# Performance work log

Measured on AMD Instinct MI355X. Metric: run time of the kernel, lower is better.

The kernel has to match this reference:

```python
import jax, jax.numpy as jnp
import numpy as np

B, I, H, V = 256, 512, 1024, 512


def _lstm_cell(x, h, c, W, U, b):
    # Keras LSTMCell: z = x@kernel + h@recurrent_kernel + bias, gate order i,f,g,o
    z = x @ W + h @ U + b  # [B, 4H]
    i, f, g, o = jnp.split(z, 4, axis=-1)
    i = jax.nn.sigmoid(i)
    f = jax.nn.sigmoid(f)
    g = jnp.tanh(g)
    o = jax.nn.sigmoid(o)
    c_new = f * c + i * g
    h_new = o * jnp.tanh(c_new)
    return h_new, c_new


def setup_inputs() -> dict:
    key = jax.random.key(0)
    ks = jax.random.split(key, 16)
    s_in = 1.0 / np.sqrt(I)
    s_h = 1.0 / np.sqrt(H)
    inp = {
        'x': jax.random.normal(ks[0], (B, I), jnp.float32),
        'h0': jax.random.normal(ks[1], (B, H), jnp.float32) * 0.1,
        'c0': jax.random.normal(ks[2], (B, H), jnp.float32) * 0.1,
        'h1': jax.random.normal(ks[3], (B, H), jnp.float32) * 0.1,
        'c1': jax.random.normal(ks[4], (B, H), jnp.float32) * 0.1,
        'h2': jax.random.normal(ks[5], (B, H), jnp.float32) * 0.1,
        'c2': jax.random.normal(ks[6], (B, H), jnp.float32) * 0.1,
        'W0': jax.random.normal(ks[7], (I, 4 * H), jnp.float32) * s_in,
        'U0': jax.random.normal(ks[8], (H, 4 * H), jnp.float32) * s_h,
        'b0': jnp.zeros((4 * H,), jnp.float32),
        'W1': jax.random.normal(ks[9], (H, 4 * H), jnp.float32) * s_h,
        'U1': jax.random.normal(ks[10], (H, 4 * H), jnp.float32) * s_h,
        'b1': jnp.zeros((4 * H,), jnp.float32),
        'W2': jax.random.normal(ks[11], (H, 4 * H), jnp.float32) * s_h,
        'U2': jax.random.normal(ks[12], (H, 4 * H), jnp.float32) * s_h,
        'b2': jnp.zeros((4 * H,), jnp.float32),
        'Wp': jax.random.normal(ks[13], (H, V), jnp.float32) * s_h,
        'bp': jnp.zeros((V,), jnp.float32),
    }
    return inp


def reference(x, h0, c0, h1, c1, h2, c2, W0, U0, b0, W1, U1, b1, W2, U2, b2, Wp, bp):
    # Stacked LSTM cells: output of each cell feeds the next
    h0n, c0n = _lstm_cell(x, h0, c0, W0, U0, b0)
    h1n, c1n = _lstm_cell(h0n, h1, c1, W1, U1, b1)
    h2n, c2n = _lstm_cell(h1n, h2, c2, W2, U2, b2)
    # Dense output projection on final cell output
    step_logits = h2n @ Wp + bp  # [B, V]
    return (step_logits, h0n, c0n, h1n, c1n, h2n, c2n)
```

## Files before the change

### kernel.cpp

```cpp
#include <hip/hip_runtime.h>


typedef __attribute__((ext_vector_type(8))) short short8_t;
typedef __attribute__((ext_vector_type(8))) unsigned short ushort8_t;
typedef __attribute__((ext_vector_type(4))) unsigned short ushort4_t;
typedef __attribute__((ext_vector_type(4))) float f32x4;

__device__ __forceinline__ unsigned short f2bf(float f) {
    union { float f; unsigned u; } v; v.f = f;
    unsigned r = v.u + 0x7FFFu + ((v.u >> 16) & 1u);
    return (unsigned short)(r >> 16);
}

#define KT 64

__global__ __launch_bounds__(512, 2)
void gemm32(const unsigned short* __restrict__ A1, const float* __restrict__ W1, int K1,
            const unsigned short* __restrict__ A2, const float* __restrict__ W2,
            int N, int Ktot, int nsplit, float* __restrict__ zp)
{
    __shared__ unsigned short Al0[256 * KT];
    __shared__ unsigned short Al1[256 * KT];
    __shared__ unsigned short Wl0[32 * KT];
    __shared__ unsigned short Wl1[32 * KT];

    const int tid  = threadIdx.x;
    const int lane = tid & 63;
    const int w    = tid >> 6;
    const int lg   = lane >> 4;
    const int lr   = lane & 15;
    const int bid  = blockIdx.x;
    const int kb   = bid & (nsplit - 1);
    const int ns   = bid >> (nsplit - 1);
    const int n0   = ns * 32;
    const int m0   = w * 32;
    const int klen = Ktot >> (nsplit - 1);
    const int kbeg = kb * klen;
    const int nt   = klen >> 6;

    const int wkr = tid >> 3;
    const int wcq = tid & 7;

    ushort8_t paA[4], paB[4];
    f32x4     pwA,   pwB;

    f32x4 acc00 = {0,0,0,0}, acc01 = {0,0,0,0}, acc10 = {0,0,0,0}, acc11 = {0,0,0,0};

    auto issue = [&](int t, ushort8_t (&pa)[4], f32x4& pw) {
        int k0 = kbeg + t * KT;
        const unsigned short* A; const float* Wm; int ldA, krel;
        if (k0 < K1) { A = A1; Wm = W1; ldA = K1;        krel = k0; }
        else         { A = A2; Wm = W2; ldA = Ktot - K1; krel = k0 - K1; }
#pragma unroll
        for (int it = 0; it < 4; ++it) {
            int c = tid + it * 512;
            int row = c >> 3, cc = c & 7;
            pa[it] = *(const ushort8_t*)(A + (size_t)row * ldA + krel + cc * 8);
        }
        pw = *(const f32x4*)(Wm + (size_t)(krel + wkr) * N + n0 + wcq * 4);
    };

    auto stage = [&](ushort8_t (&pa)[4], f32x4& pw,
                     unsigned short* al, unsigned short* wl) {
#pragma unroll
        for (int it = 0; it < 4; ++it) {
            int c = tid + it * 512;
            int row = c >> 3, cc = c & 7;
            *(ushort8_t*)(al + row * KT + ((cc ^ (row & 7)) << 3)) = pa[it];
        }
        unsigned short bs[4] = { f2bf(pw[0]), f2bf(pw[1]), f2bf(pw[2]), f2bf(pw[3]) };
        int kch = wkr >> 3, kwi = wkr & 7;
#pragma unroll
        for (int j = 0; j < 4; ++j) {
            int n = wcq * 4 + j;
            wl[n * KT + ((kch ^ (n & 7)) << 3) + kwi] = bs[j];
        }
    };

    auto compute = [&](const unsigned short* al, const unsigned short* wl) {
#pragma unroll
        for (int ks = 0; ks < 2; ++ks) {
            int ch = ks * 4 + lg;
            int nb0 = lr, nb1 = 16 + lr;
            short8_t b0f = *(const short8_t*)(wl + nb0 * KT + ((ch ^ (nb0 & 7)) << 3));
            short8_t b1f = *(const short8_t*)(wl + nb1 * KT + ((ch ^ (nb1 & 7)) << 3));
            int r0 = m0 + lr, r1 = m0 + 16 + lr;
            short8_t a0f = *(const short8_t*)(al + r0 * KT + ((ch ^ (r0 & 7)) << 3));
            short8_t a1f = *(const short8_t*)(al + r1 * KT + ((ch ^ (r1 & 7)) << 3));
            acc00 = __builtin_amdgcn_mfma_f32_16x16x32_bf16(a0f, b0f, acc00, 0, 0, 0);
            acc01 = __builtin_amdgcn_mfma_f32_16x16x32_bf16(a0f, b1f, acc01, 0, 0, 0);
            acc10 = __builtin_amdgcn_mfma_f32_16x16x32_bf16(a1f, b0f, acc10, 0, 0, 0);
            acc11 = __builtin_amdgcn_mfma_f32_16x16x32_bf16(a1f, b1f, acc11, 0, 0, 0);
        }
    };

    issue(0, paA, pwA);
    stage(paA, pwA, Al0, Wl0);
    issue(1, paB, pwB);
    __syncthreads();

    for (int t = 0; t < nt; t += 2) {
        if (t + 2 < nt) issue(t + 2, paA, pwA);
        stage(paB, pwB, Al1, Wl1);
        compute(Al0, Wl0);
        __syncthreads();
        if (t + 3 < nt) issue(t + 3, paB, pwB);
        if (t + 2 < nt) stage(paA, pwA, Al0, Wl0);
        compute(Al1, Wl1);
        __syncthreads();
    }

    float* zrow = zp + (size_t)kb * 256 * N;
#pragma unroll
    for (int r = 0; r < 4; ++r) {
        int ma = m0 + lg * 4 + r;
        int mb = ma + 16;
        zrow[(size_t)ma * N + n0 + lr]      = acc00[r];
        zrow[(size_t)ma * N + n0 + 16 + lr] = acc01[r];
        zrow[(size_t)mb * N + n0 + lr]      = acc10[r];
        zrow[(size_t)mb * N + n0 + 16 + lr] = acc11[r];
    }
}

__global__ __launch_bounds__(256)
void lstm_gates(const float* __restrict__ zp0, const float* __restrict__ zp1,
                const float* __restrict__ bias, const float* __restrict__ c_old,
                float* __restrict__ h_out, float* __restrict__ c_out,
                unsigned short* __restrict__ h_bf)
{
    int t = blockIdx.x * 256 + threadIdx.x;
    int b = t >> 8;
    int n = (t & 255) << 2;
    const float* z0 = zp0 + (size_t)b * 4096;
    f32x4 iv = *(const f32x4*)(z0 + n);
    f32x4 fv = *(const f32x4*)(z0 + 1024 + n);
    f32x4 gv = *(const f32x4*)(z0 + 2048 + n);
    f32x4 ov = *(const f32x4*)(z0 + 3072 + n);
    if (zp1) {
        const float* z1 = zp1 + (size_t)b * 4096;
        iv += *(const f32x4*)(z1 + n);
        fv += *(const f32x4*)(z1 + 1024 + n);
        gv += *(const f32x4*)(z1 + 2048 + n);
        ov += *(const f32x4*)(z1 + 3072 + n);
    }
    iv += *(const f32x4*)(bias + n);
    fv += *(const f32x4*)(bias + 1024 + n);
    gv += *(const f32x4*)(bias + 2048 + n);
    ov += *(const f32x4*)(bias + 3072 + n);
    f32x4 cv = *(const f32x4*)(c_old + (size_t)b * 1024 + n);

    f32x4 hn, cn;
    ushort4_t hb;
#pragma unroll
    for (int j = 0; j < 4; ++j) {
        float ii = 1.f / (1.f + __expf(-iv[j]));
        float ff = 1.f / (1.f + __expf(-fv[j]));
        float gg = tanhf(gv[j]);
        float oo = 1.f / (1.f + __expf(-ov[j]));
        float c2 = ff * cv[j] + ii * gg;
        cn[j] = c2;
        float h2 = oo * tanhf(c2);
        hn[j] = h2;
        hb[j] = f2bf(h2);
    }
    *(f32x4*)(c_out + (size_t)b * 1024 + n) = cn;
    *(f32x4*)(h_out + (size_t)b * 1024 + n) = hn;
    *(ushort4_t*)(h_bf + (size_t)b * 1024 + n) = hb;
}

__global__ __launch_bounds__(256)
void finalize_proj(const float* __restrict__ zp0, const float* __restrict__ zp1,
                   const float* __restrict__ bp, float* __restrict__ logits)
{
    int t = blockIdx.x * 256 + threadIdx.x;
    int i = t * 4;
    f32x4 v = *(const f32x4*)(zp0 + i);
    if (zp1) v += *(const f32x4*)(zp1 + i);
    v += *(const f32x4*)(bp + (i & 511));
    *(f32x4*)(logits + i) = v;
}

__global__ __launch_bounds__(256)
void pack_bf16(const float* __restrict__ x,  const float* __restrict__ h0,
               const float* __restrict__ h1, const float* __restrict__ h2,
               unsigned short* __restrict__ xb,  unsigned short* __restrict__ h0b,
               unsigned short* __restrict__ h1b, unsigned short* __restrict__ h2b)
{
    int t = blockIdx.x * 256 + threadIdx.x;
    const float* src; unsigned short* dst; int off;
    if (t < 32768)       { src = x;  dst = xb;  off = t; }
    else if (t < 98304)  { src = h0; dst = h0b; off = t - 32768; }
    else if (t < 163840) { src = h1; dst = h1b; off = t - 98304; }
    else                 { src = h2; dst = h2b; off = t - 163840; }
    f32x4 v = *(const f32x4*)(src + (size_t)off * 4);
    ushort4_t o;
#pragma unroll
    for (int j = 0; j < 4; ++j) o[j] = f2bf(v[j]);
    *(ushort4_t*)(dst + (size_t)off * 4) = o;
}

extern "C" void kernel_launch(void* const* d_in, const int* in_sizes, int n_in,
                              void* d_out, int out_size, void* d_ws, size_t ws_size,
                              hipStream_t stream)
{
    const float* x  = (const float*)d_in[0];
    const float* h0 = (const float*)d_in[1];
    const float* c0 = (const float*)d_in[2];
    const float* h1 = (const float*)d_in[3];
    const float* c1 = (const float*)d_in[4];
    const float* h2 = (const float*)d_in[5];
    const float* c2 = (const float*)d_in[6];
    const float* W0 = (const float*)d_in[7];
    const float* U0 = (const float*)d_in[8];
    const float* b0 = (const float*)d_in[9];
    const float* W1 = (const float*)d_in[10];
    const float* U1 = (const float*)d_in[11];
    const float* b1 = (const float*)d_in[12];
    const float* W2 = (const float*)d_in[13];
    const float* U2 = (const float*)d_in[14];
    const float* b2 = (const float*)d_in[15];
    const float* Wp = (const float*)d_in[16];
    const float* bp = (const float*)d_in[17];

    float* out    = (float*)d_out;
    float* logits = out;
    float* h0n = out + 131072;
    float* c0n = h0n + 262144;
    float* h1n = c0n + 262144;
    float* c1n = h1n + 262144;
    float* h2n = c1n + 262144;
    float* c2n = h2n + 262144;

    const size_t need2 = 8388608ull + 262144ull + 6ull * 524288ull;
    const int nsplit = (ws_size >= need2) ? 2 : 1;
    const size_t zbytes = (size_t)nsplit * 4194304ull;

    char* ws = (char*)d_ws;
    float*          zp   = (float*)ws;
    unsigned short* xb   = (unsigned short*)(ws + zbytes);
    unsigned short* h0b  = (unsigned short*)(ws + zbytes + 262144);
    unsigned short* h1b  = (unsigned short*)(ws + zbytes + 262144 + 524288);
    unsigned short* h2b  = (unsigned short*)(ws + zbytes + 262144 + 2*524288);
    unsigned short* h0nb = (unsigned short*)(ws + zbytes + 262144 + 3*524288);
    unsigned short* h1nb = (unsigned short*)(ws + zbytes + 262144 + 4*524288);
    unsigned short* h2nb = (unsigned short*)(ws + zbytes + 262144 + 5*524288);

    const float* zp1  = (nsplit == 2) ? zp + 1048576 : nullptr;
    const float* zpp1 = (nsplit == 2) ? zp + 131072  : nullptr;

    pack_bf16<<<896, 256, 0, stream>>>(x, h0, h1, h2, xb, h0b, h1b, h2b);

    gemm32<<<128 * nsplit, 512, 0, stream>>>(xb, W0, 512, h0b, U0, 4096, 1536, nsplit, zp);
    lstm_gates<<<256, 256, 0, stream>>>(zp, zp1, b0, c0, h0n, c0n, h0nb);

    gemm32<<<128 * nsplit, 512, 0, stream>>>(h0nb, W1, 1024, h1b, U1, 4096, 2048, nsplit, zp);
    lstm_gates<<<256, 256, 0, stream>>>(zp, zp1, b1, c1, h1n, c1n, h1nb);

    gemm32<<<128 * nsplit, 512, 0, stream>>>(h1nb, W2, 1024, h2b, U2, 4096, 2048, nsplit, zp);
    lstm_gates<<<256, 256, 0, stream>>>(zp, zp1, b2, c2, h2n, c2n, h2nb);

    gemm32<<<16 * nsplit, 512, 0, stream>>>(h2nb, Wp, 1024,
                                            (const unsigned short*)nullptr,
                                            (const float*)nullptr, 512, 1024, nsplit, zp);
    finalize_proj<<<128, 256, 0, stream>>>(zp, zpp1, bp, logits);
}
```

Measured before the change: 75.79 us.

## Widen GEMM N-tile to 64, deepen register prefetch, allow 4-way split-K

```diff
diff --git a/kernel.cpp b/kernel.cpp
--- a/kernel.cpp
+++ b/kernel.cpp
@@ -13,40 +13,43 @@
 }
 
 #define KT 64
-
-__global__ __launch_bounds__(512, 2)
-void gemm32(const unsigned short* __restrict__ A1, const float* __restrict__ W1, int K1,
+#define BN 64
+
+__global__ __launch_bounds__(512, 1)
+void gemm64(const unsigned short* __restrict__ A1, const float* __restrict__ W1, int K1,
             const unsigned short* __restrict__ A2, const float* __restrict__ W2,
-            int N, int Ktot, int nsplit, float* __restrict__ zp)
-{
-    __shared__ unsigned short Al0[256 * KT];
-    __shared__ unsigned short Al1[256 * KT];
-    __shared__ unsigned short Wl0[32 * KT];
-    __shared__ unsigned short Wl1[32 * KT];
+            int N, int Ktot, int lgs, float* __restrict__ zp)
+{
+    __shared__ unsigned short Al[2][256 * KT];
+    __shared__ unsigned short Wl[2][BN * KT];
 
     const int tid  = threadIdx.x;
     const int lane = tid & 63;
     const int w    = tid >> 6;
     const int lg   = lane >> 4;
     const int lr   = lane & 15;
-    const int bid  = blockIdx.x;
-    const int kb   = bid & (nsplit - 1);
-    const int ns   = bid >> (nsplit - 1);
-    const int n0   = ns * 32;
+    const int nsplit = 1 << lgs;
+    const int kb   = blockIdx.x & (nsplit - 1);
+    const int ns   = blockIdx.x >> lgs;
+    const int n0   = ns * BN;
     const int m0   = w * 32;
-    const int klen = Ktot >> (nsplit - 1);
+    const int klen = Ktot >> lgs;
     const int kbeg = kb * klen;
     const int nt   = klen >> 6;
 
-    const int wkr = tid >> 3;
-    const int wcq = tid & 7;
-
-    ushort8_t paA[4], paB[4];
-    f32x4     pwA,   pwB;
-
-    f32x4 acc00 = {0,0,0,0}, acc01 = {0,0,0,0}, acc10 = {0,0,0,0}, acc11 = {0,0,0,0};
-
-    auto issue = [&](int t, ushort8_t (&pa)[4], f32x4& pw) {
+    const int wr = tid >> 3;
+    const int wq = tid & 7;
+
+    ushort8_t pa0[4], pa1[4], pa2[4], pa3[4];
+    f32x4     pw0[2], pw1[2], pw2[2], pw3[2];
+
+    f32x4 acc[2][4];
+#pragma unroll
+    for (int i = 0; i < 2; ++i)
+#pragma unroll
+        for (int j = 0; j < 4; ++j) acc[i][j] = f32x4{0.f, 0.f, 0.f, 0.f};
+
+    auto issue = [&](int t, ushort8_t (&pa)[4], f32x4 (&pw)[2]) {
         int k0 = kbeg + t * KT;
         const unsigned short* A; const float* Wm; int ldA, krel;
         if (k0 < K1) { A = A1; Wm = W1; ldA = K1;        krel = k0; }
@@ -57,10 +60,12 @@
             int row = c >> 3, cc = c & 7;
             pa[it] = *(const ushort8_t*)(A + (size_t)row * ldA + krel + cc * 8);
         }
-        pw = *(const f32x4*)(Wm + (size_t)(krel + wkr) * N + n0 + wcq * 4);
+        const float* wrow = Wm + (size_t)(krel + wr) * N + n0;
+        pw[0] = *(const f32x4*)(wrow + wq * 4);
+        pw[1] = *(const f32x4*)(wrow + (wq + 8) * 4);
     };
 
-    auto stage = [&](ushort8_t (&pa)[4], f32x4& pw,
+    auto stage = [&](ushort8_t (&pa)[4], f32x4 (&pw)[2],
                      unsigned short* al, unsigned short* wl) {
 #pragma unroll
         for (int it = 0; it < 4; ++it) {
@@ -68,12 +73,15 @@
             int row = c >> 3, cc = c & 7;
             *(ushort8_t*)(al + row * KT + ((cc ^ (row & 7)) << 3)) = pa[it];
         }
-        unsigned short bs[4] = { f2bf(pw[0]), f2bf(pw[1]), f2bf(pw[2]), f2bf(pw[3]) };
-        int kch = wkr >> 3, kwi = wkr & 7;
-#pragma unroll
-        for (int j = 0; j < 4; ++j) {
-            int n = wcq * 4 + j;
-            wl[n * KT + ((kch ^ (n & 7)) << 3) + kwi] = bs[j];
+        int kch = wr >> 3, kwi = wr & 7;
+#pragma unroll
+        for (int p = 0; p < 2; ++p) {
+            int qq = wq + p * 8;
+#pragma unroll
+            for (int j = 0; j < 4; ++j) {
+                int n = qq * 4 + j;
+                wl[n * KT + ((kch ^ (n & 7)) << 3) + kwi] = f2bf(pw[p][j]);
+            }
         }
     };
 
@@ -81,49 +89,58 @@
 #pragma unroll
         for (int ks = 0; ks < 2; ++ks) {
             int ch = ks * 4 + lg;
-            int nb0 = lr, nb1 = 16 + lr;
-            short8_t b0f = *(const short8_t*)(wl + nb0 * KT + ((ch ^ (nb0 & 7)) << 3));
-            short8_t b1f = *(const short8_t*)(wl + nb1 * KT + ((ch ^ (nb1 & 7)) << 3));
-            int r0 = m0 + lr, r1 = m0 + 16 + lr;
-            short8_t a0f = *(const short8_t*)(al + r0 * KT + ((ch ^ (r0 & 7)) << 3));
-            short8_t a1f = *(const short8_t*)(al + r1 * KT + ((ch ^ (r1 & 7)) << 3));
-            acc00 = __builtin_amdgcn_mfma_f32_16x16x32_bf16(a0f, b0f, acc00, 0, 0, 0);
-            acc01 = __builtin_amdgcn_mfma_f32_16x16x32_bf16(a0f, b1f, acc01, 0, 0, 0);
-            acc10 = __builtin_amdgcn_mfma_f32_16x16x32_bf16(a1f, b0f, acc10, 0, 0, 0);
-            acc11 = __builtin_amdgcn_mfma_f32_16x16x32_bf16(a1f, b1f, acc11, 0, 0, 0);
+            int r0 = m0 + lr, r1 = r0 + 16;
+            short8_t a0 = *(const short8_t*)(al + r0 * KT + ((ch ^ (r0 & 7)) << 3));
+            short8_t a1 = *(const short8_t*)(al + r1 * KT + ((ch ^ (r1 & 7)) << 3));
+#pragma unroll
+            for (int n4 = 0; n4 < 4; ++n4) {
+                int nb = n4 * 16 + lr;
+                short8_t b = *(const short8_t*)(wl + nb * KT + ((ch ^ (nb & 7)) << 3));
+                acc[0][n4] = __builtin_amdgcn_mfma_f32_16x16x32_bf16(a0, b, acc[0][n4], 0, 0, 0);
+                acc[1][n4] = __builtin_amdgcn_mfma_f32_16x16x32_bf16(a1, b, acc[1][n4], 0, 0, 0);
+            }
         }
     };
 
-    issue(0, paA, pwA);
-    stage(paA, pwA, Al0, Wl0);
-    issue(1, paB, pwB);
+    if (0 < nt) issue(0, pa0, pw0);
+    if (1 < nt) issue(1, pa1, pw1);
+    if (2 < nt) issue(2, pa2, pw2);
+    stage(pa0, pw0, Al[0], Wl[0]);
     __syncthreads();
 
-    for (int t = 0; t < nt; t += 2) {
-        if (t + 2 < nt) issue(t + 2, paA, pwA);
-        stage(paB, pwB, Al1, Wl1);
-        compute(Al0, Wl0);
-        __syncthreads();
-        if (t + 3 < nt) issue(t + 3, paB, pwB);
-        if (t + 2 < nt) stage(paA, pwA, Al0, Wl0);
-        compute(Al1, Wl1);
+    for (int t = 0; t < nt; t += 4) {
+        if (t + 3 < nt) issue(t + 3, pa3, pw3);
+        if (t + 1 < nt) stage(pa1, pw1, Al[1], Wl[1]);
+        compute(Al[0], Wl[0]);
+        __syncthreads();
+        if (t + 4 < nt) issue(t + 4, pa0, pw0);
+        if (t + 2 < nt) stage(pa2, pw2, Al[0], Wl[0]);
+        if (t + 1 < nt) compute(Al[1], Wl[1]);
+        __syncthreads();
+        if (t + 5 < nt) issue(t + 5, pa1, pw1);
+        if (t + 3 < nt) stage(pa3, pw3, Al[1], Wl[1]);
+        if (t + 2 < nt) compute(Al[0], Wl[0]);
+        __syncthreads();
+        if (t + 6 < nt) issue(t + 6, pa2, pw2);
+        if (t + 4 < nt) stage(pa0, pw0, Al[0], Wl[0]);
+        if (t + 3 < nt) compute(Al[1], Wl[1]);
         __syncthreads();
     }
 
-    float* zrow = zp + (size_t)kb * 256 * N;
-#pragma unroll
-    for (int r = 0; r < 4; ++r) {
-        int ma = m0 + lg * 4 + r;
-        int mb = ma + 16;
-        zrow[(size_t)ma * N + n0 + lr]      = acc00[r];
-        zrow[(size_t)ma * N + n0 + 16 + lr] = acc01[r];
-        zrow[(size_t)mb * N + n0 + lr]      = acc10[r];
-        zrow[(size_t)mb * N + n0 + 16 + lr] = acc11[r];
-    }
+    float* zq = zp + (size_t)kb * 256 * N;
+#pragma unroll
+    for (int ms = 0; ms < 2; ++ms)
+#pragma unroll
+        for (int n4 = 0; n4 < 4; ++n4)
+#pragma unroll
+            for (int r = 0; r < 4; ++r) {
+                int row = m0 + ms * 16 + lg * 4 + r;
+                zq[(size_t)row * N + n0 + n4 * 16 + lr] = acc[ms][n4][r];
+            }
 }
 
 __global__ __launch_bounds__(256)
-void lstm_gates(const float* __restrict__ zp0, const float* __restrict__ zp1,
+void lstm_gates(const float* __restrict__ zp, int nsplit,
                 const float* __restrict__ bias, const float* __restrict__ c_old,
                 float* __restrict__ h_out, float* __restrict__ c_out,
                 unsigned short* __restrict__ h_bf)
@@ -131,22 +148,17 @@
     int t = blockIdx.x * 256 + threadIdx.x;
     int b = t >> 8;
     int n = (t & 255) << 2;
-    const float* z0 = zp0 + (size_t)b * 4096;
-    f32x4 iv = *(const f32x4*)(z0 + n);
-    f32x4 fv = *(const f32x4*)(z0 + 1024 + n);
-    f32x4 gv = *(const f32x4*)(z0 + 2048 + n);
-    f32x4 ov = *(const f32x4*)(z0 + 3072 + n);
-    if (zp1) {
-        const float* z1 = zp1 + (size_t)b * 4096;
-        iv += *(const f32x4*)(z1 + n);
-        fv += *(const f32x4*)(z1 + 1024 + n);
-        gv += *(const f32x4*)(z1 + 2048 + n);
-        ov += *(const f32x4*)(z1 + 3072 + n);
+    f32x4 iv = *(const f32x4*)(bias + n);
+    f32x4 fv = *(const f32x4*)(bias + 1024 + n);
+    f32x4 gv = *(const f32x4*)(bias + 2048 + n);
+    f32x4 ov = *(const f32x4*)(bias + 3072 + n);
+    for (int kb = 0; kb < nsplit; ++kb) {
+        const float* z = zp + (size_t)kb * 1048576 + (size_t)b * 4096;
+        iv += *(const f32x4*)(z + n);
+        fv += *(const f32x4*)(z + 1024 + n);
+        gv += *(const f32x4*)(z + 2048 + n);
+        ov += *(const f32x4*)(z + 3072 + n);
     }
-    iv += *(const f32x4*)(bias + n);
-    fv += *(const f32x4*)(bias + 1024 + n);
-    gv += *(const f32x4*)(bias + 2048 + n);
-    ov += *(const f32x4*)(bias + 3072 + n);
     f32x4 cv = *(const f32x4*)(c_old + (size_t)b * 1024 + n);
 
     f32x4 hn, cn;
@@ -169,14 +181,14 @@
 }
 
 __global__ __launch_bounds__(256)
-void finalize_proj(const float* __restrict__ zp0, const float* __restrict__ zp1,
+void finalize_proj(const float* __restrict__ zp, int nsplit,
                    const float* __restrict__ bp, float* __restrict__ logits)
 {
     int t = blockIdx.x * 256 + threadIdx.x;
     int i = t * 4;
-    f32x4 v = *(const f32x4*)(zp0 + i);
-    if (zp1) v += *(const f32x4*)(zp1 + i);
-    v += *(const f32x4*)(bp + (i & 511));
+    f32x4 v = *(const f32x4*)(bp + (i & 511));
+    for (int kb = 0; kb < nsplit; ++kb)
+        v += *(const f32x4*)(zp + (size_t)kb * 131072 + i);
     *(f32x4*)(logits + i) = v;
 }
 
@@ -231,8 +243,9 @@
     float* h2n = c1n + 262144;
     float* c2n = h2n + 262144;
 
-    const size_t need2 = 8388608ull + 262144ull + 6ull * 524288ull;
-    const int nsplit = (ws_size >= need2) ? 2 : 1;
+    const size_t need4 = 16777216ull + 262144ull + 6ull * 524288ull;
+    const int nsplit = (ws_size >= need4) ? 4 : 2;
+    const int lgs    = (nsplit == 4) ? 2 : 1;
     const size_t zbytes = (size_t)nsplit * 4194304ull;
 
     char* ws = (char*)d_ws;
@@ -245,22 +258,19 @@
     unsigned short* h1nb = (unsigned short*)(ws + zbytes + 262144 + 4*524288);
     unsigned short* h2nb = (unsigned short*)(ws + zbytes + 262144 + 5*524288);
 
-    const float* zp1  = (nsplit == 2) ? zp + 1048576 : nullptr;
-    const float* zpp1 = (nsplit == 2) ? zp + 131072  : nullptr;
-
     pack_bf16<<<896, 256, 0, stream>>>(x, h0, h1, h2, xb, h0b, h1b, h2b);
 
-    gemm32<<<128 * nsplit, 512, 0, stream>>>(xb, W0, 512, h0b, U0, 4096, 1536, nsplit, zp);
-    lstm_gates<<<256, 256, 0, stream>>>(zp, zp1, b0, c0, h0n, c0n, h0nb);
-
-    gemm32<<<128 * nsplit, 512, 0, stream>>>(h0nb, W1, 1024, h1b, U1, 4096, 2048, nsplit, zp);
-    lstm_gates<<<256, 256, 0, stream>>>(zp, zp1, b1, c1, h1n, c1n, h1nb);
-
-    gemm32<<<128 * nsplit, 512, 0, stream>>>(h1nb, W2, 1024, h2b, U2, 4096, 2048, nsplit, zp);
-    lstm_gates<<<256, 256, 0, stream>>>(zp, zp1, b2, c2, h2n, c2n, h2nb);
-
-    gemm32<<<16 * nsplit, 512, 0, stream>>>(h2nb, Wp, 1024,
-                                            (const unsigned short*)nullptr,
-                                            (const float*)nullptr, 512, 1024, nsplit, zp);
-    finalize_proj<<<128, 256, 0, stream>>>(zp, zpp1, bp, logits);
-}
+    gemm64<<<64 * nsplit, 512, 0, stream>>>(xb, W0, 512, h0b, U0, 4096, 1536, lgs, zp);
+    lstm_gates<<<256, 256, 0, stream>>>(zp, nsplit, b0, c0, h0n, c0n, h0nb);
+
+    gemm64<<<64 * nsplit, 512, 0, stream>>>(h0nb, W1, 1024, h1b, U1, 4096, 2048, lgs, zp);
+    lstm_gates<<<256, 256, 0, stream>>>(zp, nsplit, b1, c1, h1n, c1n, h1nb);
+
+    gemm64<<<64 * nsplit, 512, 0, stream>>>(h1nb, W2, 1024, h2b, U2, 4096, 2048, lgs, zp);
+    lstm_gates<<<256, 256, 0, stream>>>(zp, nsplit, b2, c2, h2n, c2n, h2nb);
+
+    gemm64<<<8 * nsplit, 512, 0, stream>>>(h2nb, Wp, 1024,
+                                           (const unsigned short*)nullptr,
+                                           (const float*)nullptr, 512, 1024, lgs, zp);
+    finalize_proj<<<128, 256, 0, stream>>>(zp, nsplit, bp, logits);
+}
```

Result: slower. 82.22 us (+8.5%).

## Hoist all recurrent-state GEMMs into one multi-piece launch with deeper split-K

Applied to the files above, without the earlier changes.

```diff
diff --git a/kernel.cpp b/kernel.cpp
--- a/kernel.cpp
+++ b/kernel.cpp
@@ -13,28 +13,49 @@
 }
 
 #define KT 64
-
-__global__ __launch_bounds__(512, 2)
-void gemm32(const unsigned short* __restrict__ A1, const float* __restrict__ W1, int K1,
-            const unsigned short* __restrict__ A2, const float* __restrict__ W2,
-            int N, int Ktot, int nsplit, float* __restrict__ zp)
+#define BN 32
+
+struct GemmPiece {
+    const unsigned short* A;
+    const float*          W;
+    float*                Z;
+    int K;
+    int lgs;
+    int bstart;
+};
+struct GemmDesc { GemmPiece p[4]; int np; int N; };
+
+__global__ __launch_bounds__(512, 4)
+void gemm_multi(GemmDesc d)
 {
     __shared__ unsigned short Al0[256 * KT];
     __shared__ unsigned short Al1[256 * KT];
-    __shared__ unsigned short Wl0[32 * KT];
-    __shared__ unsigned short Wl1[32 * KT];
+    __shared__ unsigned short Wl0[BN * KT];
+    __shared__ unsigned short Wl1[BN * KT];
+
+    const int bid = blockIdx.x;
+    int pi = 0;
+#pragma unroll
+    for (int i = 1; i < 4; ++i)
+        if (i < d.np && bid >= d.p[i].bstart) pi = i;
+    const unsigned short* __restrict__ A = d.p[pi].A;
+    const float* __restrict__ W = d.p[pi].W;
+    const int K   = d.p[pi].K;
+    const int lgs = d.p[pi].lgs;
+    const int N   = d.N;
+    const int lb  = bid - d.p[pi].bstart;
+    const int nsplit = 1 << lgs;
+    const int kb  = lb & (nsplit - 1);
+    const int ns  = lb >> lgs;
 
     const int tid  = threadIdx.x;
     const int lane = tid & 63;
     const int w    = tid >> 6;
     const int lg   = lane >> 4;
     const int lr   = lane & 15;
-    const int bid  = blockIdx.x;
-    const int kb   = bid & (nsplit - 1);
-    const int ns   = bid >> (nsplit - 1);
-    const int n0   = ns * 32;
+    const int n0   = ns * BN;
     const int m0   = w * 32;
-    const int klen = Ktot >> (nsplit - 1);
+    const int klen = K >> lgs;
     const int kbeg = kb * klen;
     const int nt   = klen >> 6;
 
@@ -48,16 +69,13 @@
 
     auto issue = [&](int t, ushort8_t (&pa)[4], f32x4& pw) {
         int k0 = kbeg + t * KT;
-        const unsigned short* A; const float* Wm; int ldA, krel;
-        if (k0 < K1) { A = A1; Wm = W1; ldA = K1;        krel = k0; }
-        else         { A = A2; Wm = W2; ldA = Ktot - K1; krel = k0 - K1; }
 #pragma unroll
         for (int it = 0; it < 4; ++it) {
             int c = tid + it * 512;
             int row = c >> 3, cc = c & 7;
-            pa[it] = *(const ushort8_t*)(A + (size_t)row * ldA + krel + cc * 8);
+            pa[it] = *(const ushort8_t*)(A + (size_t)row * K + k0 + cc * 8);
         }
-        pw = *(const f32x4*)(Wm + (size_t)(krel + wkr) * N + n0 + wcq * 4);
+        pw = *(const f32x4*)(W + (size_t)(k0 + wkr) * N + n0 + wcq * 4);
     };
 
     auto stage = [&](ushort8_t (&pa)[4], f32x4& pw,
@@ -110,7 +128,7 @@
         __syncthreads();
     }
 
-    float* zrow = zp + (size_t)kb * 256 * N;
+    float* zrow = d.p[pi].Z + (size_t)kb * 256 * N;
 #pragma unroll
     for (int r = 0; r < 4; ++r) {
         int ma = m0 + lg * 4 + r;
@@ -123,7 +141,8 @@
 }
 
 __global__ __launch_bounds__(256)
-void lstm_gates(const float* __restrict__ zp0, const float* __restrict__ zp1,
+void lstm_gates(const float* __restrict__ pz1, int n1,
+                const float* __restrict__ pz2, int n2,
                 const float* __restrict__ bias, const float* __restrict__ c_old,
                 float* __restrict__ h_out, float* __restrict__ c_out,
                 unsigned short* __restrict__ h_bf)
@@ -131,22 +150,24 @@
     int t = blockIdx.x * 256 + threadIdx.x;
     int b = t >> 8;
     int n = (t & 255) << 2;
-    const float* z0 = zp0 + (size_t)b * 4096;
-    f32x4 iv = *(const f32x4*)(z0 + n);
-    f32x4 fv = *(const f32x4*)(z0 + 1024 + n);
-    f32x4 gv = *(const f32x4*)(z0 + 2048 + n);
-    f32x4 ov = *(const f32x4*)(z0 + 3072 + n);
-    if (zp1) {
-        const float* z1 = zp1 + (size_t)b * 4096;
-        iv += *(const f32x4*)(z1 + n);
-        fv += *(const f32x4*)(z1 + 1024 + n);
-        gv += *(const f32x4*)(z1 + 2048 + n);
-        ov += *(const f32x4*)(z1 + 3072 + n);
-    }
-    iv += *(const f32x4*)(bias + n);
-    fv += *(const f32x4*)(bias + 1024 + n);
-    gv += *(const f32x4*)(bias + 2048 + n);
-    ov += *(const f32x4*)(bias + 3072 + n);
+    f32x4 iv = *(const f32x4*)(bias + n);
+    f32x4 fv = *(const f32x4*)(bias + 1024 + n);
+    f32x4 gv = *(const f32x4*)(bias + 2048 + n);
+    f32x4 ov = *(const f32x4*)(bias + 3072 + n);
+    for (int i = 0; i < n1; ++i) {
+        const float* z = pz1 + (size_t)i * 1048576 + (size_t)b * 4096;
+        iv += *(const f32x4*)(z + n);
+        fv += *(const f32x4*)(z + 1024 + n);
+        gv += *(const f32x4*)(z + 2048 + n);
+        ov += *(const f32x4*)(z + 3072 + n);
+    }
+    for (int i = 0; i < n2; ++i) {
+        const float* z = pz2 + (size_t)i * 1048576 + (size_t)b * 4096;
+        iv += *(const f32x4*)(z + n);
+        fv += *(const f32x4*)(z + 1024 + n);
+        gv += *(const f32x4*)(z + 2048 + n);
+        ov += *(const f32x4*)(z + 3072 + n);
+    }
     f32x4 cv = *(const f32x4*)(c_old + (size_t)b * 1024 + n);
 
     f32x4 hn, cn;
@@ -169,14 +190,14 @@
 }
 
 __global__ __launch_bounds__(256)
-void finalize_proj(const float* __restrict__ zp0, const float* __restrict__ zp1,
+void finalize_proj(const float* __restrict__ zp, int nsplit,
                    const float* __restrict__ bp, float* __restrict__ logits)
 {
     int t = blockIdx.x * 256 + threadIdx.x;
     int i = t * 4;
-    f32x4 v = *(const f32x4*)(zp0 + i);
-    if (zp1) v += *(const f32x4*)(zp1 + i);
-    v += *(const f32x4*)(bp + (i & 511));
+    f32x4 v = *(const f32x4*)(bp + (i & 511));
+    for (int kb = 0; kb < nsplit; ++kb)
+        v += *(const f32x4*)(zp + (size_t)kb * 131072 + i);
     *(f32x4*)(logits + i) = v;
 }
 
@@ -231,36 +252,93 @@
     float* h2n = c1n + 262144;
     float* c2n = h2n + 262144;
 
-    const size_t need2 = 8388608ull + 262144ull + 6ull * 524288ull;
-    const int nsplit = (ws_size >= need2) ? 2 : 1;
-    const size_t zbytes = (size_t)nsplit * 4194304ull;
-
-    char* ws = (char*)d_ws;
-    float*          zp   = (float*)ws;
-    unsigned short* xb   = (unsigned short*)(ws + zbytes);
-    unsigned short* h0b  = (unsigned short*)(ws + zbytes + 262144);
-    unsigned short* h1b  = (unsigned short*)(ws + zbytes + 262144 + 524288);
-    unsigned short* h2b  = (unsigned short*)(ws + zbytes + 262144 + 2*524288);
-    unsigned short* h0nb = (unsigned short*)(ws + zbytes + 262144 + 3*524288);
-    unsigned short* h1nb = (unsigned short*)(ws + zbytes + 262144 + 4*524288);
-    unsigned short* h2nb = (unsigned short*)(ws + zbytes + 262144 + 5*524288);
-
-    const float* zp1  = (nsplit == 2) ? zp + 1048576 : nullptr;
-    const float* zpp1 = (nsplit == 2) ? zp + 131072  : nullptr;
+    const size_t SLOT = 1048576;
+    const size_t bf_bytes = 262144ull + 6ull * 524288ull;
+    const size_t need6 = 6ull * 4194304ull + bf_bytes;
+    const size_t need4 = 4ull * 4194304ull + bf_bytes;
+    const int nslots = (ws_size >= need6) ? 6 : (ws_size >= need4) ? 4 : 2;
+
+    float* S = (float*)d_ws;
+    auto S_at = [&](int i) { return S + (size_t)i * SLOT; };
+    unsigned short* bufs = (unsigned short*)(S + (size_t)nslots * SLOT);
+    unsigned short* xb   = bufs;
+    unsigned short* h0b  = bufs + 131072;
+    unsigned short* h1b  = h0b + 262144;
+    unsigned short* h2b  = h1b + 262144;
+    unsigned short* h0nb = h2b + 262144;
+    unsigned short* h1nb = h0nb + 262144;
+    unsigned short* h2nb = h1nb + 262144;
 
     pack_bf16<<<896, 256, 0, stream>>>(x, h0, h1, h2, xb, h0b, h1b, h2b);
 
-    gemm32<<<128 * nsplit, 512, 0, stream>>>(xb, W0, 512, h0b, U0, 4096, 1536, nsplit, zp);
-    lstm_gates<<<256, 256, 0, stream>>>(zp, zp1, b0, c0, h0n, c0n, h0nb);
-
-    gemm32<<<128 * nsplit, 512, 0, stream>>>(h0nb, W1, 1024, h1b, U1, 4096, 2048, nsplit, zp);
-    lstm_gates<<<256, 256, 0, stream>>>(zp, zp1, b1, c1, h1n, c1n, h1nb);
-
-    gemm32<<<128 * nsplit, 512, 0, stream>>>(h1nb, W2, 1024, h2b, U2, 4096, 2048, nsplit, zp);
-    lstm_gates<<<256, 256, 0, stream>>>(zp, zp1, b2, c2, h2n, c2n, h2nb);
-
-    gemm32<<<16 * nsplit, 512, 0, stream>>>(h2nb, Wp, 1024,
-                                            (const unsigned short*)nullptr,
-                                            (const float*)nullptr, 512, 1024, nsplit, zp);
-    finalize_proj<<<128, 256, 0, stream>>>(zp, zpp1, bp, logits);
-}
+    if (nslots >= 4) {
+        float* Su1 = S_at(nslots == 6 ? 4 : 2);
+        float* Su2 = S_at(nslots == 6 ? 5 : 3);
+
+        GemmDesc mega;
+        mega.p[0] = { xb,  W0, S_at(0), 512,  0, 0   };
+        mega.p[1] = { h0b, U0, S_at(1), 1024, 0, 128 };
+        mega.p[2] = { h1b, U1, Su1,     1024, 0, 256 };
+        mega.p[3] = { h2b, U2, Su2,     1024, 0, 384 };
+        mega.np = 4; mega.N = 4096;
+        gemm_multi<<<512, 512, 0, stream>>>(mega);
+        lstm_gates<<<256, 256, 0, stream>>>(S_at(0), 2, nullptr, 0, b0, c0,
+                                            h0n, c0n, h0nb);
+
+        const int lgsG = (nslots == 6) ? 2 : 1;
+        GemmDesc g1;
+        g1.p[0] = { h0nb, W1, S_at(0), 1024, lgsG, 0 };
+        g1.p[1] = g1.p[2] = g1.p[3] = g1.p[0];
+        g1.np = 1; g1.N = 4096;
+        gemm_multi<<<128 << lgsG, 512, 0, stream>>>(g1);
+        lstm_gates<<<256, 256, 0, stream>>>(S_at(0), 1 << lgsG, Su1, 1, b1, c1,
+                                            h1n, c1n, h1nb);
+
+        GemmDesc g2;
+        g2.p[0] = { h1nb, W2, S_at(0), 1024, lgsG, 0 };
+        g2.p[1] = g2.p[2] = g2.p[3] = g2.p[0];
+        g2.np = 1; g2.N = 4096;
+        gemm_multi<<<128 << lgsG, 512, 0, stream>>>(g2);
+        lstm_gates<<<256, 256, 0, stream>>>(S_at(0), 1 << lgsG, Su2, 1, b2, c2,
+                                            h2n, c2n, h2nb);
+
+        float* Sp = (nslots == 6) ? S_at(4) : S_at(2);
+        GemmDesc gp;
+        gp.p[0] = { h2nb, Wp, Sp, 1024, 2, 0 };
+        gp.p[1] = gp.p[2] = gp.p[3] = gp.p[0];
+        gp.np = 1; gp.N = 512;
+        gemm_multi<<<64, 512, 0, stream>>>(gp);
+        finalize_proj<<<128, 256, 0, stream>>>(Sp, 4, bp, logits);
+    } else {
+        GemmDesc m1;
+        m1.p[0] = { xb,  W0, S_at(0), 512,  0, 0   };
+        m1.p[1] = { h0b, U0, S_at(1), 1024, 0, 128 };
+        m1.p[2] = m1.p[3] = m1.p[1];
+        m1.np = 2; m1.N = 4096;
+        gemm_multi<<<256, 512, 0, stream>>>(m1);
+        lstm_gates<<<256, 256, 0, stream>>>(S_at(0), 2, nullptr, 0, b0, c0,
+                                            h0n, c0n, h0nb);
+        GemmDesc m2;
+        m2.p[0] = { h0nb, W1, S_at(0), 1024, 0, 0   };
+        m2.p[1] = { h1b,  U1, S_at(1), 1024, 0, 128 };
+        m2.p[2] = m2.p[3] = m2.p[1];
+        m2.np = 2; m2.N = 4096;
+        gemm_multi<<<256, 512, 0, stream>>>(m2);
+        lstm_gates<<<256, 256, 0, stream>>>(S_at(0), 2, nullptr, 0, b1, c1,
+                                            h1n, c1n, h1nb);
+        GemmDesc m3;
+        m3.p[0] = { h1nb, W2, S_at(0), 1024, 0, 0   };
+        m3.p[1] = { h2b,  U2, S_at(1), 1024, 0, 128 };
+        m3.p[2] = m3.p[3] = m3.p[1];
+        m3.np = 2; m3.N = 4096;
+        gemm_multi<<<256, 512, 0, stream>>>(m3);
+        lstm_gates<<<256, 256, 0, stream>>>(S_at(0), 2, nullptr, 0, b2, c2,
+                                            h2n, c2n, h2nb);
+        GemmDesc gp;
+        gp.p[0] = { h2nb, Wp, S_at(1), 1024, 2, 0 };
+        gp.p[1] = gp.p[2] = gp.p[3] = gp.p[0];
+        gp.np = 1; gp.N = 512;
+        gemm_multi<<<64, 512, 0, stream>>>(gp);
+        finalize_proj<<<128, 256, 0, stream>>>(S_at(1), 4, bp, logits);
+    }
+}
```

Result: slower. 78.12 us (+3.1%).

## Raise split-K to four for LSTM GEMMs and eight for projection

Applied to the files above, without the earlier changes.

```diff
diff --git a/kernel.cpp b/kernel.cpp
--- a/kernel.cpp
+++ b/kernel.cpp
@@ -13,28 +13,30 @@
 }
 
 #define KT 64
-
-__global__ __launch_bounds__(512, 2)
+#define BN 32
+#define SLOT 1048576
+
+__global__ __launch_bounds__(512, 4)
 void gemm32(const unsigned short* __restrict__ A1, const float* __restrict__ W1, int K1,
             const unsigned short* __restrict__ A2, const float* __restrict__ W2,
-            int N, int Ktot, int nsplit, float* __restrict__ zp)
+            int N, int Ktot, int lgs, float* __restrict__ zp)
 {
     __shared__ unsigned short Al0[256 * KT];
     __shared__ unsigned short Al1[256 * KT];
-    __shared__ unsigned short Wl0[32 * KT];
-    __shared__ unsigned short Wl1[32 * KT];
+    __shared__ unsigned short Wl0[BN * KT];
+    __shared__ unsigned short Wl1[BN * KT];
 
     const int tid  = threadIdx.x;
     const int lane = tid & 63;
     const int w    = tid >> 6;
     const int lg   = lane >> 4;
     const int lr   = lane & 15;
-    const int bid  = blockIdx.x;
-    const int kb   = bid & (nsplit - 1);
-    const int ns   = bid >> (nsplit - 1);
-    const int n0   = ns * 32;
+    const int nsplit = 1 << lgs;
+    const int kb   = blockIdx.x & (nsplit - 1);
+    const int ns   = blockIdx.x >> lgs;
+    const int n0   = ns * BN;
     const int m0   = w * 32;
-    const int klen = Ktot >> (nsplit - 1);
+    const int klen = Ktot >> lgs;
     const int kbeg = kb * klen;
     const int nt   = klen >> 6;
 
@@ -42,7 +44,7 @@
     const int wcq = tid & 7;
 
     ushort8_t paA[4], paB[4];
-    f32x4     pwA,   pwB;
+    f32x4     pwA = {0,0,0,0}, pwB = {0,0,0,0};
 
     f32x4 acc00 = {0,0,0,0}, acc01 = {0,0,0,0}, acc10 = {0,0,0,0}, acc11 = {0,0,0,0};
 
@@ -94,21 +96,27 @@
         }
     };
 
+#define BAR() do { asm volatile("s_waitcnt lgkmcnt(0)" ::: "memory"); \
+                   __builtin_amdgcn_s_barrier(); } while (0)
+
     issue(0, paA, pwA);
     stage(paA, pwA, Al0, Wl0);
-    issue(1, paB, pwB);
-    __syncthreads();
+    if (1 < nt) issue(1, paB, pwB);
+    BAR();
 
     for (int t = 0; t < nt; t += 2) {
         if (t + 2 < nt) issue(t + 2, paA, pwA);
-        stage(paB, pwB, Al1, Wl1);
+        if (t + 1 < nt) stage(paB, pwB, Al1, Wl1);
         compute(Al0, Wl0);
-        __syncthreads();
-        if (t + 3 < nt) issue(t + 3, paB, pwB);
-        if (t + 2 < nt) stage(paA, pwA, Al0, Wl0);
-        compute(Al1, Wl1);
-        __syncthreads();
-    }
+        BAR();
+        if (t + 1 < nt) {
+            if (t + 3 < nt) issue(t + 3, paB, pwB);
+            if (t + 2 < nt) stage(paA, pwA, Al0, Wl0);
+            compute(Al1, Wl1);
+            BAR();
+        }
+    }
+#undef BAR
 
     float* zrow = zp + (size_t)kb * 256 * N;
 #pragma unroll
@@ -123,7 +131,7 @@
 }
 
 __global__ __launch_bounds__(256)
-void lstm_gates(const float* __restrict__ zp0, const float* __restrict__ zp1,
+void lstm_gates(const float* __restrict__ zp, int nsplit,
                 const float* __restrict__ bias, const float* __restrict__ c_old,
                 float* __restrict__ h_out, float* __restrict__ c_out,
                 unsigned short* __restrict__ h_bf)
@@ -131,22 +139,17 @@
     int t = blockIdx.x * 256 + threadIdx.x;
     int b = t >> 8;
     int n = (t & 255) << 2;
-    const float* z0 = zp0 + (size_t)b * 4096;
-    f32x4 iv = *(const f32x4*)(z0 + n);
-    f32x4 fv = *(const f32x4*)(z0 + 1024 + n);
-    f32x4 gv = *(const f32x4*)(z0 + 2048 + n);
-    f32x4 ov = *(const f32x4*)(z0 + 3072 + n);
-    if (zp1) {
-        const float* z1 = zp1 + (size_t)b * 4096;
-        iv += *(const f32x4*)(z1 + n);
-        fv += *(const f32x4*)(z1 + 1024 + n);
-        gv += *(const f32x4*)(z1 + 2048 + n);
-        ov += *(const f32x4*)(z1 + 3072 + n);
-    }
-    iv += *(const f32x4*)(bias + n);
-    fv += *(const f32x4*)(bias + 1024 + n);
-    gv += *(const f32x4*)(bias + 2048 + n);
-    ov += *(const f32x4*)(bias + 3072 + n);
+    f32x4 iv = *(const f32x4*)(bias + n);
+    f32x4 fv = *(const f32x4*)(bias + 1024 + n);
+    f32x4 gv = *(const f32x4*)(bias + 2048 + n);
+    f32x4 ov = *(const f32x4*)(bias + 3072 + n);
+    for (int kb = 0; kb < nsplit; ++kb) {
+        const float* z = zp + (size_t)kb * SLOT + (size_t)b * 4096;
+        iv += *(const f32x4*)(z + n);
+        fv += *(const f32x4*)(z + 1024 + n);
+        gv += *(const f32x4*)(z + 2048 + n);
+        ov += *(const f32x4*)(z + 3072 + n);
+    }
     f32x4 cv = *(const f32x4*)(c_old + (size_t)b * 1024 + n);
 
     f32x4 hn, cn;
@@ -169,14 +172,14 @@
 }
 
 __global__ __launch_bounds__(256)
-void finalize_proj(const float* __restrict__ zp0, const float* __restrict__ zp1,
+void finalize_proj(const float* __restrict__ zp, int nsplit,
                    const float* __restrict__ bp, float* __restrict__ logits)
 {
     int t = blockIdx.x * 256 + threadIdx.x;
     int i = t * 4;
-    f32x4 v = *(const f32x4*)(zp0 + i);
-    if (zp1) v += *(const f32x4*)(zp1 + i);
-    v += *(const f32x4*)(bp + (i & 511));
+    f32x4 v = *(const f32x4*)(bp + (i & 511));
+    for (int kb = 0; kb < nsplit; ++kb)
+        v += *(const f32x4*)(zp + (size_t)kb * 131072 + i);
     *(f32x4*)(logits + i) = v;
 }
 
@@ -231,8 +234,10 @@
     float* h2n = c1n + 262144;
     float* c2n = h2n + 262144;
 
-    const size_t need2 = 8388608ull + 262144ull + 6ull * 524288ull;
-    const int nsplit = (ws_size >= need2) ? 2 : 1;
+    const size_t need4 = 16777216ull + 262144ull + 6ull * 524288ull;
+    const size_t need2 = 8388608ull  + 262144ull + 6ull * 524288ull;
+    const int lgs    = (ws_size >= need4) ? 2 : (ws_size >= need2) ? 1 : 0;
+    const int nsplit = 1 << lgs;
     const size_t zbytes = (size_t)nsplit * 4194304ull;
 
     char* ws = (char*)d_ws;
@@ -245,22 +250,19 @@
     unsigned short* h1nb = (unsigned short*)(ws + zbytes + 262144 + 4*524288);
     unsigned short* h2nb = (unsigned short*)(ws + zbytes + 262144 + 5*524288);
 
-    const float* zp1  = (nsplit == 2) ? zp + 1048576 : nullptr;
-    const float* zpp1 = (nsplit == 2) ? zp + 131072  : nullptr;
-
     pack_bf16<<<896, 256, 0, stream>>>(x, h0, h1, h2, xb, h0b, h1b, h2b);
 
-    gemm32<<<128 * nsplit, 512, 0, stream>>>(xb, W0, 512, h0b, U0, 4096, 1536, nsplit, zp);
-    lstm_gates<<<256, 256, 0, stream>>>(zp, zp1, b0, c0, h0n, c0n, h0nb);
-
-    gemm32<<<128 * nsplit, 512, 0, stream>>>(h0nb, W1, 1024, h1b, U1, 4096, 2048, nsplit, zp);
-    lstm_gates<<<256, 256, 0, stream>>>(zp, zp1, b1, c1, h1n, c1n, h1nb);
-
-    gemm32<<<128 * nsplit, 512, 0, stream>>>(h1nb, W2, 1024, h2b, U2, 4096, 2048, nsplit, zp);
-    lstm_gates<<<256, 256, 0, stream>>>(zp, zp1, b2, c2, h2n, c2n, h2nb);
-
-    gemm32<<<16 * nsplit, 512, 0, stream>>>(h2nb, Wp, 1024,
-                                            (const unsigned short*)nullptr,
-                                            (const float*)nullptr, 512, 1024, nsplit, zp);
-    finalize_proj<<<128, 256, 0, stream>>>(zp, zpp1, bp, logits);
-}
+    gemm32<<<128 * nsplit, 512, 0, stream>>>(xb, W0, 512, h0b, U0, 4096, 1536, lgs, zp);
+    lstm_gates<<<256, 256, 0, stream>>>(zp, nsplit, b0, c0, h0n, c0n, h0nb);
+
+    gemm32<<<128 * nsplit, 512, 0, stream>>>(h0nb, W1, 1024, h1b, U1, 4096, 2048, lgs, zp);
+    lstm_gates<<<256, 256, 0, stream>>>(zp, nsplit, b1, c1, h1n, c1n, h1nb);
+
+    gemm32<<<128 * nsplit, 512, 0, stream>>>(h1nb, W2, 1024, h2b, U2, 4096, 2048, lgs, zp);
+    lstm_gates<<<256, 256, 0, stream>>>(zp, nsplit, b2, c2, h2n, c2n, h2nb);
+
+    gemm32<<<16 * 8, 512, 0, stream>>>(h2nb, Wp, 1024,
+                                       (const unsigned short*)nullptr,
+                                       (const float*)nullptr, 512, 1024, 3, zp);
+    finalize_proj<<<128, 256, 0, stream>>>(zp, 8, bp, logits);
+}
```

Measured after the change: 77.57 us. +2.3%, slower.
